# Optimization experiments

Hardware: AMD Instinct MI355X
Metric: run time of the kernel (lower is better)

The kernel has to match this reference:

```python
import jax, jax.numpy as jnp
import numpy as np

B, T, D, H = 2, 2048, 2048, 16
HD = D // H


def setup_inputs() -> dict:
    key = jax.random.key(0)
    ks = jax.random.split(key, 6)
    s = 1.0 / np.sqrt(D)
    return {
        "x": jax.random.normal(ks[0], (B, T, D), dtype=jnp.float32),
        "Wq": jax.random.normal(ks[1], (D, D), dtype=jnp.float32) * s,
        "Wk": jax.random.normal(ks[2], (D, D), dtype=jnp.float32) * s,
        "Wv": jax.random.normal(ks[3], (D, D), dtype=jnp.float32) * s,
        "Wo": jax.random.normal(ks[4], (D, D), dtype=jnp.float32) * s,
        "bo": jnp.zeros((D,), dtype=jnp.float32),
    }


def reference(x, Wq, Wk, Wv, Wo, bo):
    b, t, d = x.shape
    # projections (torch Linear: x @ W.T)
    q = (x @ Wq.T).reshape(b, t, H, HD).transpose(0, 2, 1, 3)  # [B,H,T,HD]
    k = (x @ Wk.T).reshape(b, t, H, HD).transpose(0, 2, 1, 3)
    v = (x @ Wv.T).reshape(b, t, H, HD).transpose(0, 2, 1, 3)
    scores = jnp.einsum('bhid,bhjd->bhij', q, k) / np.sqrt(HD)  # [B,H,T,T]
    causal = jnp.tril(jnp.ones((t, t), dtype=bool))
    scores = jnp.where(causal[None, None], scores, -jnp.inf)
    attn = jax.nn.softmax(scores, axis=-1)
    out = jnp.einsum('bhij,bhjd->bhid', attn, v)  # [B,H,T,HD]
    out = out.transpose(0, 2, 1, 3).reshape(b, t, d)
    return out @ Wo.T + bo
```

## Files before the change

### kernel.cpp

```cpp
#include <hip/hip_runtime.h>
#include <hip/hip_bf16.h>

#define T_ 2048
#define D_ 2048
#define H_ 16
#define HD_ 128

typedef __hip_bfloat16 bf16;
using bf16x8 = __attribute__((ext_vector_type(8))) short;
using f32x4  = __attribute__((ext_vector_type(4))) float;

#define GLL16(g, l) __builtin_amdgcn_global_load_lds( \
    (const __attribute__((address_space(1))) void*)(g), \
    (__attribute__((address_space(3))) void*)(l), 16, 0, 0)

__device__ __forceinline__ f32x4 mfma16(bf16x8 a, bf16x8 b, f32x4 c) {
    return __builtin_amdgcn_mfma_f32_16x16x32_bf16(a, b, c, 0, 0, 0);
}

__global__ __launch_bounds__(256) void cast6(
    const float* __restrict__ s0, const float* __restrict__ s1,
    const float* __restrict__ s2, const float* __restrict__ s3,
    const float* __restrict__ s4, const float* __restrict__ s5,
    bf16* __restrict__ dst)
{
    int z = blockIdx.y;
    const float* s = (z == 0) ? s0 : (z == 1) ? s1 : (z == 2) ? s2
                   : (z == 3) ? s3 : (z == 4) ? s4 : s5;
    long i = ((long)blockIdx.x * 256 + threadIdx.x) * 8;
    float4 a = *(const float4*)(s + i);
    float4 b = *(const float4*)(s + i + 4);
    union { bf16 h[8]; int4 v; } u;
    u.h[0] = __float2bfloat16(a.x); u.h[1] = __float2bfloat16(a.y);
    u.h[2] = __float2bfloat16(a.z); u.h[3] = __float2bfloat16(a.w);
    u.h[4] = __float2bfloat16(b.x); u.h[5] = __float2bfloat16(b.y);
    u.h[6] = __float2bfloat16(b.z); u.h[7] = __float2bfloat16(b.w);
    *(int4*)(dst + (long)z * 4194304 + i) = u.v;
}

__global__ __launch_bounds__(256) void gemm_qkv(
    const bf16* __restrict__ xb,
    const bf16* __restrict__ wq, const bf16* __restrict__ wk, const bf16* __restrict__ wv,
    bf16* __restrict__ Qo, bf16* __restrict__ Ko, bf16* __restrict__ Vo)
{
    __shared__ bf16 As[128*32];
    __shared__ bf16 Bs[128*32];
    int z = blockIdx.z;
    const bf16* W = (z == 0) ? wq : (z == 1) ? wk : wv;
    bf16* out = (z == 0) ? Qo : (z == 1) ? Ko : Vo;
    int bn = blockIdx.x, bm = blockIdx.y;
    int tid = threadIdx.x, lane = tid & 63, w = tid >> 6;
    int wm = w >> 1, wn = w & 1;
    const bf16* Abase = xb + (long)bm * 128 * D_;
    const bf16* Bbase = W  + (long)bn * 128 * D_;
    int srow = w*16 + (lane >> 2);
    int scol = (lane & 3) * 8;

    f32x4 acc[4][4];
    #pragma unroll
    for (int i = 0; i < 4; ++i)
        #pragma unroll
        for (int j = 0; j < 4; ++j) acc[i][j] = f32x4{0.f,0.f,0.f,0.f};

    for (int kt = 0; kt < D_/32; ++kt) {
        const bf16* Ag = Abase + kt*32;
        const bf16* Bg = Bbase + kt*32;
        GLL16(Ag + (long)srow*D_ + scol,        As + w*512);
        GLL16(Ag + (long)(srow+64)*D_ + scol,   As + 2048 + w*512);
        GLL16(Bg + (long)srow*D_ + scol,        Bs + w*512);
        GLL16(Bg + (long)(srow+64)*D_ + scol,   Bs + 2048 + w*512);
        __syncthreads();
        bf16x8 af[4], bfr[4];
        #pragma unroll
        for (int mt = 0; mt < 4; ++mt)
            af[mt] = *(const bf16x8*)&As[(wm*64 + mt*16 + (lane & 15))*32 + (lane >> 4)*8];
        #pragma unroll
        for (int nt = 0; nt < 4; ++nt)
            bfr[nt] = *(const bf16x8*)&Bs[(wn*64 + nt*16 + (lane & 15))*32 + (lane >> 4)*8];
        #pragma unroll
        for (int mt = 0; mt < 4; ++mt)
            #pragma unroll
            for (int nt = 0; nt < 4; ++nt)
                acc[mt][nt] = mfma16(af[mt], bfr[nt], acc[mt][nt]);
        __syncthreads();
    }
    int mlo = bm*128 + wm*64;
    int nlo = bn*128 + wn*64;
    #pragma unroll
    for (int mt = 0; mt < 4; ++mt) {
        #pragma unroll
        for (int nt = 0; nt < 4; ++nt) {
            int n = nlo + nt*16 + (lane & 15);
            int h = n >> 7, hd = n & 127;
            #pragma unroll
            for (int r = 0; r < 4; ++r) {
                int m = mlo + mt*16 + (lane >> 4)*4 + r;
                int b = m >> 11, t = m & 2047;
                out[(((long)(b*H_ + h))*T_ + t)*HD_ + hd] = __float2bfloat16(acc[mt][nt][r]);
            }
        }
    }
}

__global__ __launch_bounds__(256) void attn(
    const bf16* __restrict__ Qm, const bf16* __restrict__ Km, const bf16* __restrict__ Vm,
    bf16* __restrict__ Om)
{
    __shared__ bf16 Ks[64*136];
    __shared__ bf16 Vt[128*72];
    __shared__ bf16 Ps[128*72];
    int bm = 15 - (blockIdx.x >> 5);
    int bh = blockIdx.x & 31;
    int tid = threadIdx.x, lane = tid & 63, w = tid >> 6;
    const float c1 = 0.12754012780914427f;
    const float c2 = 23.083120654223414f;
    const bf16* Qb = Qm + (long)bh*T_*HD_;
    const bf16* Kb = Km + (long)bh*T_*HD_;
    const bf16* Vb = Vm + (long)bh*T_*HD_;
    int m0 = bm*128 + w*32;

    bf16x8 qf[2][4];
    #pragma unroll
    for (int mt = 0; mt < 2; ++mt)
        #pragma unroll
        for (int ks = 0; ks < 4; ++ks)
            qf[mt][ks] = *(const bf16x8*)(Qb + (long)(m0 + mt*16 + (lane & 15))*HD_ + ks*32 + (lane >> 4)*8);

    bf16x8 onesB;
    {
        short v1 = ((lane & 15) == 0) ? (short)0x3F80 : (short)0;
        #pragma unroll
        for (int jj = 0; jj < 8; ++jj) onesB[jj] = v1;
    }

    f32x4 oacc[2][8];
    f32x4 lacc[2];
    #pragma unroll
    for (int mt = 0; mt < 2; ++mt) {
        lacc[mt] = f32x4{0.f,0.f,0.f,0.f};
        #pragma unroll
        for (int dt = 0; dt < 8; ++dt) oacc[mt][dt] = f32x4{0.f,0.f,0.f,0.f};
    }

    int krow = (tid >> 4);
    int kcg  = tid & 15;
    int njt = 2*bm + 2;

    bf16x8 kreg[4], vreg[4];
    #pragma unroll
    for (int i = 0; i < 4; ++i) {
        kreg[i] = *(const bf16x8*)(Kb + (long)(i*16 + krow)*HD_ + kcg*8);
        vreg[i] = *(const bf16x8*)(Vb + (long)lane*HD_ + (w + i*4)*8);
    }

    for (int j = 0; j < njt; ++j) {
        int j0 = j*64;
        __syncthreads();
        #pragma unroll
        for (int i = 0; i < 4; ++i)
            *(bf16x8*)&Ks[(i*16 + krow)*136 + kcg*8] = kreg[i];
        #pragma unroll
        for (int i = 0; i < 4; ++i) {
            int dg = w + i*4;
            union { bf16 h[8]; bf16x8 v; } u;
            u.v = vreg[i];
            #pragma unroll
            for (int jj = 0; jj < 8; ++jj)
                Vt[(dg*8 + jj)*72 + lane] = u.h[jj];
        }
        __syncthreads();

        if (j + 1 < njt) {
            int jn0 = j0 + 64;
            #pragma unroll
            for (int i = 0; i < 4; ++i) {
                kreg[i] = *(const bf16x8*)(Kb + (long)(jn0 + i*16 + krow)*HD_ + kcg*8);
                vreg[i] = *(const bf16x8*)(Vb + (long)(jn0 + lane)*HD_ + (w + i*4)*8);
            }
        }

        bool anyv  = (j0 <= m0 + 31);
        if (anyv) {
            bool bmask = (j0 + 63 > m0);
            f32x4 s[2][4];
            #pragma unroll
            for (int mt = 0; mt < 2; ++mt)
                #pragma unroll
                for (int nt = 0; nt < 4; ++nt) s[mt][nt] = f32x4{0.f,0.f,0.f,0.f};
            #pragma unroll
            for (int ks = 0; ks < 4; ++ks) {
                bf16x8 kf[4];
                #pragma unroll
                for (int nt = 0; nt < 4; ++nt)
                    kf[nt] = *(const bf16x8*)&Ks[(nt*16 + (lane & 15))*136 + ks*32 + (lane >> 4)*8];
                #pragma unroll
                for (int mt = 0; mt < 2; ++mt)
                    #pragma unroll
                    for (int nt = 0; nt < 4; ++nt)
                        s[mt][nt] = mfma16(qf[mt][ks], kf[nt], s[mt][nt]);
            }
            #pragma unroll
            for (int mt = 0; mt < 2; ++mt) {
                #pragma unroll
                for (int nt = 0; nt < 4; ++nt) {
                    int n = j0 + nt*16 + (lane & 15);
                    #pragma unroll
                    for (int r = 0; r < 4; ++r) {
                        float x = s[mt][nt][r] * c1 - c2;
                        if (bmask) {
                            int mg = m0 + mt*16 + (lane >> 4)*4 + r;
                            x = (n <= mg) ? x : -1e30f;
                        }
                        float p = exp2f(x);
                        int prow = w*32 + mt*16 + (lane >> 4)*4 + r;
                        Ps[prow*72 + nt*16 + (lane & 15)] = __float2bfloat16(p);
                    }
                }
            }
            #pragma unroll
            for (int kn = 0; kn < 2; ++kn) {
                bf16x8 pf[2], vf[8];
                #pragma unroll
                for (int mt = 0; mt < 2; ++mt)
                    pf[mt] = *(const bf16x8*)&Ps[(w*32 + mt*16 + (lane & 15))*72 + kn*32 + (lane >> 4)*8];
                #pragma unroll
                for (int dt = 0; dt < 8; ++dt)
                    vf[dt] = *(const bf16x8*)&Vt[(dt*16 + (lane & 15))*72 + kn*32 + (lane >> 4)*8];
                #pragma unroll
                for (int mt = 0; mt < 2; ++mt)
                    lacc[mt] = mfma16(pf[mt], onesB, lacc[mt]);
                #pragma unroll
                for (int mt = 0; mt < 2; ++mt)
                    #pragma unroll
                    for (int dt = 0; dt < 8; ++dt)
                        oacc[mt][dt] = mfma16(pf[mt], vf[dt], oacc[mt][dt]);
            }
        }
    }
    int b = bh >> 4, h = bh & 15;
    #pragma unroll
    for (int mt = 0; mt < 2; ++mt) {
        #pragma unroll
        for (int r = 0; r < 4; ++r) {
            float l = __shfl(lacc[mt][r], lane & 48, 64);
            float inv = 1.f / l;
            int t = m0 + mt*16 + (lane >> 4)*4 + r;
            #pragma unroll
            for (int dt = 0; dt < 8; ++dt) {
                int d = dt*16 + (lane & 15);
                Om[((long)(b*T_ + t))*D_ + h*HD_ + d] = __float2bfloat16(oacc[mt][dt][r] * inv);
            }
        }
    }
}

__global__ __launch_bounds__(256) void gemm_out(
    const bf16* __restrict__ Ab, const bf16* __restrict__ Wob,
    const float* __restrict__ bo, float* __restrict__ out)
{
    __shared__ bf16 As[128*32];
    __shared__ bf16 Bs[128*32];
    int bn = blockIdx.x, bm = blockIdx.y;
    int tid = threadIdx.x, lane = tid & 63, w = tid >> 6;
    int wm = w >> 1, wn = w & 1;
    const bf16* Abase = Ab  + (long)bm * 128 * D_;
    const bf16* Bbase = Wob + (long)bn * 128 * D_;
    int srow = w*16 + (lane >> 2);
    int scol = (lane & 3) * 8;

    f32x4 acc[4][4];
    #pragma unroll
    for (int i = 0; i < 4; ++i)
        #pragma unroll
        for (int j = 0; j < 4; ++j) acc[i][j] = f32x4{0.f,0.f,0.f,0.f};

    for (int kt = 0; kt < D_/32; ++kt) {
        const bf16* Ag = Abase + kt*32;
        const bf16* Bg = Bbase + kt*32;
        GLL16(Ag + (long)srow*D_ + scol,        As + w*512);
        GLL16(Ag + (long)(srow+64)*D_ + scol,   As + 2048 + w*512);
        GLL16(Bg + (long)srow*D_ + scol,        Bs + w*512);
        GLL16(Bg + (long)(srow+64)*D_ + scol,   Bs + 2048 + w*512);
        __syncthreads();
        bf16x8 af[4], bfr[4];
        #pragma unroll
        for (int mt = 0; mt < 4; ++mt)
            af[mt] = *(const bf16x8*)&As[(wm*64 + mt*16 + (lane & 15))*32 + (lane >> 4)*8];
        #pragma unroll
        for (int nt = 0; nt < 4; ++nt)
            bfr[nt] = *(const bf16x8*)&Bs[(wn*64 + nt*16 + (lane & 15))*32 + (lane >> 4)*8];
        #pragma unroll
        for (int mt = 0; mt < 4; ++mt)
            #pragma unroll
            for (int nt = 0; nt < 4; ++nt)
                acc[mt][nt] = mfma16(af[mt], bfr[nt], acc[mt][nt]);
        __syncthreads();
    }
    int mlo = bm*128 + wm*64;
    int nlo = bn*128 + wn*64;
    #pragma unroll
    for (int mt = 0; mt < 4; ++mt) {
        #pragma unroll
        for (int nt = 0; nt < 4; ++nt) {
            int n = nlo + nt*16 + (lane & 15);
            float bias = bo[n];
            #pragma unroll
            for (int r = 0; r < 4; ++r) {
                int m = mlo + mt*16 + (lane >> 4)*4 + r;
                out[(long)m*D_ + n] = acc[mt][nt][r] + bias;
            }
        }
    }
}

extern "C" void kernel_launch(void* const* d_in, const int* in_sizes, int n_in,
                              void* d_out, int out_size, void* d_ws, size_t ws_size,
                              hipStream_t stream) {
    const float* x  = (const float*)d_in[0];
    const float* Wq = (const float*)d_in[1];
    const float* Wk = (const float*)d_in[2];
    const float* Wv = (const float*)d_in[3];
    const float* Wo = (const float*)d_in[4];
    const float* bo = (const float*)d_in[5];
    float* out = (float*)d_out;

    bf16* ws  = (bf16*)d_ws;
    bf16* xb  = ws;
    bf16* wqb = ws + 8388608L;
    bf16* wkb = ws + 12582912L;
    bf16* wvb = ws + 16777216L;
    bf16* wob = ws + 20971520L;
    bf16* Qb  = ws + 25165824L;
    bf16* Kb  = ws + 33554432L;
    bf16* Vb  = ws + 41943040L;
    bf16* Ob  = xb;

    cast6<<<dim3(2048, 6), 256, 0, stream>>>(x, x + 4194304L, Wq, Wk, Wv, Wo, ws);
    gemm_qkv<<<dim3(16, 32, 3), 256, 0, stream>>>(xb, wqb, wkb, wvb, Qb, Kb, Vb);
    attn<<<512, 256, 0, stream>>>(Qb, Kb, Vb, Ob);
    gemm_out<<<dim3(16, 32), 256, 0, stream>>>(Ob, wob, bo, out);
}
```

Measured before the change: 399.2 us.

## Add 4-stage LDS pipeline with swizzle and priority to projection GEMMs

Replaces the single-buffered load/sync/compute loop in the QKV and output projection GEMMs with a 4-deep ring of LDS buffers and three tiles prefetched ahead. Per-iteration waits use manual vmcnt counts with one barrier instead of two __syncthreads. The global-to-LDS column placement is XOR-style swizzled by row to cut LDS bank conflicts on fragment reads, and MFMA sections run at raised wave priority. LDS use grows fourfold per block (64KB), which may reduce occupancy.

```diff
diff --git a/kernel.cpp b/kernel.cpp
--- a/kernel.cpp
+++ b/kernel.cpp
@@ -38,52 +38,77 @@
     *(int4*)(dst + (long)z * 4194304 + i) = u.v;
 }
 
+
+#define STAGE(t, b) do { \
+    const bf16* Ag_ = Abase + (t)*32; \
+    const bf16* Bg_ = Bbase + (t)*32; \
+    GLL16(Ag_ + aoff0, As[b] + w*512); \
+    GLL16(Ag_ + aoff1, As[b] + 2048 + w*512); \
+    GLL16(Bg_ + aoff0, Bs[b] + w*512); \
+    GLL16(Bg_ + aoff1, Bs[b] + 2048 + w*512); \
+} while (0)
+
+#define GEMM_MAINLOOP() \
+    int tid = threadIdx.x, lane = tid & 63, w = tid >> 6; \
+    int wm = w >> 1, wn = w & 1; \
+    int srow = w*16 + (lane >> 2); \
+     \
+     \
+    int scol = ((((lane & 3) - (srow >> 1)) & 3)) * 8; \
+    long aoff0 = (long)srow * D_ + scol; \
+    long aoff1 = aoff0 + 64L * D_; \
+    f32x4 acc[4][4]; \
+    _Pragma("unroll") \
+    for (int i = 0; i < 4; ++i) \
+        _Pragma("unroll") \
+        for (int j = 0; j < 4; ++j) acc[i][j] = f32x4{0.f,0.f,0.f,0.f}; \
+    STAGE(0, 0); STAGE(1, 1); STAGE(2, 2); \
+    for (int kt = 0; kt < D_/32; ++kt) { \
+        int rem = D_/32 - 1 - kt; \
+        if (rem >= 2)      asm volatile("s_waitcnt vmcnt(8)" ::: "memory"); \
+        else if (rem == 1) asm volatile("s_waitcnt vmcnt(4)" ::: "memory"); \
+        else               asm volatile("s_waitcnt vmcnt(0)" ::: "memory"); \
+        __builtin_amdgcn_s_barrier(); \
+        asm volatile("" ::: "memory"); \
+        int cb = kt & 3; \
+        int g = lane >> 4; \
+        bf16x8 af[4], bfr[4]; \
+        _Pragma("unroll") \
+        for (int mt = 0; mt < 4; ++mt) { \
+            int r = wm*64 + mt*16 + (lane & 15); \
+            af[mt] = *(const bf16x8*)&As[cb][r*32 + (((g + (r >> 1)) & 3) * 8)]; \
+        } \
+        _Pragma("unroll") \
+        for (int nt = 0; nt < 4; ++nt) { \
+            int r = wn*64 + nt*16 + (lane & 15); \
+            bfr[nt] = *(const bf16x8*)&Bs[cb][r*32 + (((g + (r >> 1)) & 3) * 8)]; \
+        } \
+        if (kt + 3 < D_/32) { STAGE(kt + 3, (kt + 3) & 3); } \
+        __builtin_amdgcn_s_setprio(1); \
+        _Pragma("unroll") \
+        for (int mt = 0; mt < 4; ++mt) \
+            _Pragma("unroll") \
+            for (int nt = 0; nt < 4; ++nt) \
+                acc[mt][nt] = mfma16(af[mt], bfr[nt], acc[mt][nt]); \
+        __builtin_amdgcn_s_setprio(0); \
+    }
+
 __global__ __launch_bounds__(256) void gemm_qkv(
     const bf16* __restrict__ xb,
     const bf16* __restrict__ wq, const bf16* __restrict__ wk, const bf16* __restrict__ wv,
     bf16* __restrict__ Qo, bf16* __restrict__ Ko, bf16* __restrict__ Vo)
 {
-    __shared__ bf16 As[128*32];
-    __shared__ bf16 Bs[128*32];
+    __shared__ bf16 As[4][128*32];
+    __shared__ bf16 Bs[4][128*32];
     int z = blockIdx.z;
     const bf16* W = (z == 0) ? wq : (z == 1) ? wk : wv;
     bf16* out = (z == 0) ? Qo : (z == 1) ? Ko : Vo;
     int bn = blockIdx.x, bm = blockIdx.y;
-    int tid = threadIdx.x, lane = tid & 63, w = tid >> 6;
-    int wm = w >> 1, wn = w & 1;
     const bf16* Abase = xb + (long)bm * 128 * D_;
     const bf16* Bbase = W  + (long)bn * 128 * D_;
-    int srow = w*16 + (lane >> 2);
-    int scol = (lane & 3) * 8;
-
-    f32x4 acc[4][4];
-    #pragma unroll
-    for (int i = 0; i < 4; ++i)
-        #pragma unroll
-        for (int j = 0; j < 4; ++j) acc[i][j] = f32x4{0.f,0.f,0.f,0.f};
-
-    for (int kt = 0; kt < D_/32; ++kt) {
-        const bf16* Ag = Abase + kt*32;
-        const bf16* Bg = Bbase + kt*32;
-        GLL16(Ag + (long)srow*D_ + scol,        As + w*512);
-        GLL16(Ag + (long)(srow+64)*D_ + scol,   As + 2048 + w*512);
-        GLL16(Bg + (long)srow*D_ + scol,        Bs + w*512);
-        GLL16(Bg + (long)(srow+64)*D_ + scol,   Bs + 2048 + w*512);
-        __syncthreads();
-        bf16x8 af[4], bfr[4];
-        #pragma unroll
-        for (int mt = 0; mt < 4; ++mt)
-            af[mt] = *(const bf16x8*)&As[(wm*64 + mt*16 + (lane & 15))*32 + (lane >> 4)*8];
-        #pragma unroll
-        for (int nt = 0; nt < 4; ++nt)
-            bfr[nt] = *(const bf16x8*)&Bs[(wn*64 + nt*16 + (lane & 15))*32 + (lane >> 4)*8];
-        #pragma unroll
-        for (int mt = 0; mt < 4; ++mt)
-            #pragma unroll
-            for (int nt = 0; nt < 4; ++nt)
-                acc[mt][nt] = mfma16(af[mt], bfr[nt], acc[mt][nt]);
-        __syncthreads();
-    }
+
+    GEMM_MAINLOOP();
+
     int mlo = bm*128 + wm*64;
     int nlo = bn*128 + wn*64;
     #pragma unroll
@@ -258,44 +283,14 @@
     const bf16* __restrict__ Ab, const bf16* __restrict__ Wob,
     const float* __restrict__ bo, float* __restrict__ out)
 {
-    __shared__ bf16 As[128*32];
-    __shared__ bf16 Bs[128*32];
+    __shared__ bf16 As[4][128*32];
+    __shared__ bf16 Bs[4][128*32];
     int bn = blockIdx.x, bm = blockIdx.y;
-    int tid = threadIdx.x, lane = tid & 63, w = tid >> 6;
-    int wm = w >> 1, wn = w & 1;
     const bf16* Abase = Ab  + (long)bm * 128 * D_;
     const bf16* Bbase = Wob + (long)bn * 128 * D_;
-    int srow = w*16 + (lane >> 2);
-    int scol = (lane & 3) * 8;
-
-    f32x4 acc[4][4];
-    #pragma unroll
-    for (int i = 0; i < 4; ++i)
-        #pragma unroll
-        for (int j = 0; j < 4; ++j) acc[i][j] = f32x4{0.f,0.f,0.f,0.f};
-
-    for (int kt = 0; kt < D_/32; ++kt) {
-        const bf16* Ag = Abase + kt*32;
-        const bf16* Bg = Bbase + kt*32;
-        GLL16(Ag + (long)srow*D_ + scol,        As + w*512);
-        GLL16(Ag + (long)(srow+64)*D_ + scol,   As + 2048 + w*512);
-        GLL16(Bg + (long)srow*D_ + scol,        Bs + w*512);
-        GLL16(Bg + (long)(srow+64)*D_ + scol,   Bs + 2048 + w*512);
-        __syncthreads();
-        bf16x8 af[4], bfr[4];
-        #pragma unroll
-        for (int mt = 0; mt < 4; ++mt)
-            af[mt] = *(const bf16x8*)&As[(wm*64 + mt*16 + (lane & 15))*32 + (lane >> 4)*8];
-        #pragma unroll
-        for (int nt = 0; nt < 4; ++nt)
-            bfr[nt] = *(const bf16x8*)&Bs[(wn*64 + nt*16 + (lane & 15))*32 + (lane >> 4)*8];
-        #pragma unroll
-        for (int mt = 0; mt < 4; ++mt)
-            #pragma unroll
-            for (int nt = 0; nt < 4; ++nt)
-                acc[mt][nt] = mfma16(af[mt], bfr[nt], acc[mt][nt]);
-        __syncthreads();
-    }
+
+    GEMM_MAINLOOP();
+
     int mlo = bm*128 + wm*64;
     int nlo = bn*128 + wn*64;
     #pragma unroll
```

Result: faster. 390.7 us (-2.1%).
